# Kernel tuning notes

Measured on AMD Instinct MI355X. Metric: run time of the kernel, lower is better.

The kernel has to match this reference:

```python
import jax, jax.numpy as jnp
import numpy as np

# Hyperparameters (from init_kwargs)
N = 100000      # num_nodes
T = 4           # num_edge_type
E = 400000      # edges per type
C = 2           # num_channels
L = 2           # num_layers
W_IN = 128      # input feature dim
D = 64          # node_dim (w_out)
NUM_CLASS = 16
BETA = 0.5
M = 10000       # number of target nodes


def setup_inputs() -> dict:
    key = jax.random.key(0)
    ks = jax.random.split(key, 10)
    glorot = np.sqrt(6.0 / (W_IN + D))
    glorot1 = np.sqrt(6.0 / (C * D + D))
    glorot2 = np.sqrt(6.0 / (D + NUM_CLASS))
    return {
        "X": jax.random.normal(ks[0], (N, W_IN), dtype=jnp.float32),
        "edge_value": jax.random.uniform(ks[1], (T, E), dtype=jnp.float32),
        "conv_weights": 0.1 * jax.random.normal(ks[2], (L, C, T), dtype=jnp.float32),
        "Ws": jax.random.uniform(ks[3], (C, W_IN, D), minval=-glorot, maxval=glorot, dtype=jnp.float32),
        "lin1_w": jax.random.uniform(ks[4], (C * D, D), minval=-glorot1, maxval=glorot1, dtype=jnp.float32),
        "lin1_b": jnp.zeros((D,), dtype=jnp.float32),
        "lin_w": jax.random.uniform(ks[5], (D, NUM_CLASS), minval=-glorot2, maxval=glorot2, dtype=jnp.float32),
        "lin_b": jnp.zeros((NUM_CLASS,), dtype=jnp.float32),
        "edge_index": jax.random.randint(ks[6], (T, 2, E), 0, N),
        "target_x": jax.random.randint(ks[7], (M,), 0, N),
    }


def reference(X, edge_value, conv_weights, Ws, lin1_w, lin1_b, lin_w, lin_b,
              edge_index, target_x):
    # Flatten edge types into one big edge list. torch_sparse.coalesce(op='add')
    # followed by torch.sparse.mm is mathematically a duplicate-summing SpMM,
    # i.e. a segment_sum over destination rows.
    rows = edge_index[:, 0, :].reshape(-1)      # [T*E]
    cols = edge_index[:, 1, :].reshape(-1)      # [T*E]
    vals = edge_value.reshape(-1)               # [T*E]
    type_id = jnp.repeat(jnp.arange(T), E)      # [T*E] edge-type id (constant)

    # Per-channel input projections: X_ = X @ Ws[c]  -> [C, N, D]
    X_ = jnp.einsum('nf,cfd->cnd', X, Ws)
    H = X_

    for l in range(L):
        # FastGTConv: softmax over edge types per channel
        filt = jax.nn.softmax(conv_weights[l], axis=1)   # [C, T]
        newH = []
        for c in range(C):
            v = vals * filt[c, type_id]                  # [T*E] mixed edge weights
            msgs = v[:, None] * H[c][cols]               # gather + scale: [T*E, D]
            newH.append(jax.ops.segment_sum(msgs, rows, num_segments=N))
        H = jnp.stack(newH)                              # [C, N, D]

    # FastGTN tail: relu(beta*X_ + (1-beta)*H), concat channels, linear1
    Hc = jax.nn.relu(BETA * X_ + (1.0 - BETA) * H)       # [C, N, D]
    Hcat = jnp.transpose(Hc, (1, 0, 2)).reshape(N, C * D)
    H_ = Hcat @ lin1_w + lin1_b                          # [N, D]

    # FastGTNs head: logits at target nodes
    return H_[target_x] @ lin_w + lin_b                  # [M, NUM_CLASS]
```

## Files before the change

### kernel.cpp

```cpp
#include <hip/hip_runtime.h>

#define N_NODES   100000
#define T_TYPES   4
#define E_EDGES   400000
#define E4        100000
#define G_TOT     400000
#define C_CH      2
#define W_INF     128
#define DD        64
#define NUM_CLASS 16
#define BETA      0.5f
#define M_TGT     10000

#define NSB       1563
#define NSB_PAD   1568
#define SBPAD     1408
#define CHUNK_G   1024
#define NPART_BLK 391
#define PROJ_BLK  1563

static const size_t PLANE2 = (size_t)N_NODES * DD;

typedef __attribute__((ext_vector_type(8))) short short8x;
typedef __attribute__((ext_vector_type(4))) float f32x4;

__device__ __forceinline__ unsigned bf16rne(float x) {
    unsigned u = __float_as_uint(x);
    return (u + 0x7FFFu + ((u >> 16) & 1u)) >> 16;
}
__device__ __forceinline__ unsigned packbf(float a, float b) {
    return bf16rne(a) | (bf16rne(b) << 16);
}
__device__ __forceinline__ float bflo(unsigned u) { return __uint_as_float(u << 16); }
__device__ __forceinline__ float bfhi(unsigned u) { return __uint_as_float(u & 0xFFFF0000u); }

__device__ __forceinline__ void load_filter(const float* cw, int layer,
                                            float* f0, float* f1) {
    float m0 = -1e30f, m1 = -1e30f;
    #pragma unroll
    for (int t = 0; t < T_TYPES; ++t) {
        f0[t] = cw[layer * C_CH * T_TYPES + t];
        f1[t] = cw[layer * C_CH * T_TYPES + T_TYPES + t];
        m0 = fmaxf(m0, f0[t]); m1 = fmaxf(m1, f1[t]);
    }
    float s0 = 0.f, s1 = 0.f;
    #pragma unroll
    for (int t = 0; t < T_TYPES; ++t) {
        f0[t] = __expf(f0[t] - m0); s0 += f0[t];
        f1[t] = __expf(f1[t] - m1); s1 += f1[t];
    }
    #pragma unroll
    for (int t = 0; t < T_TYPES; ++t) { f0[t] /= s0; f1[t] /= s1; }
}

__global__ void prep_kernel(const float* __restrict__ Ws,
                            unsigned short* __restrict__ Wsb,
                            int* __restrict__ cursor) {
    int b = blockIdx.x;
    int tid = threadIdx.x;
    if (b < 64) {
        int idx = b * 256 + tid;
        int c   = idx >> 13;
        int rem = idx & 8191;
        int d   = rem >> 7;
        int k   = rem & 127;
        Wsb[idx] = (unsigned short)bf16rne(Ws[c * (W_INF * DD) + k * DD + d]);
    } else {
        int idx = (b - 64) * 256 + tid;
        if (idx < NSB) cursor[idx] = idx * SBPAD;
    }
}

__global__ __launch_bounds__(256) void build_proj_kernel(
        const int* __restrict__ edge_index,
        const float* __restrict__ edge_value,
        const float* __restrict__ cw,
        int* __restrict__ cursor,
        int2* __restrict__ edata2,
        const float* __restrict__ X,
        const unsigned short* __restrict__ Wsb,
        unsigned* __restrict__ Xp16) {
    __shared__ int cnt[NSB_PAD];
    __shared__ int gbase[NSB_PAD];
    int tid = threadIdx.x;

    if (blockIdx.x < NPART_BLK) {
        int p = blockIdx.x;
        for (int j = tid; j < NSB; j += 256) cnt[j] = 0;
        __syncthreads();

        float f0[T_TYPES], f1[T_TYPES];
        load_filter(cw, 0, f0, f1);

        int px[16], rk[16], bk[16];
        bool gv[4];
        #pragma unroll
        for (int g = 0; g < 4; ++g) {
            int idx = p * CHUNK_G + g * 256 + tid;
            gv[g] = idx < G_TOT;
            if (gv[g]) {
                int t = idx / E4, r = idx - t * E4;
                const int* bptr = edge_index + (size_t)t * 2 * E_EDGES;
                int4 rw = ((const int4*)bptr)[r];
                int4 cl = ((const int4*)(bptr + E_EDGES))[r];
                int tb = t << 17;
                int rr[4] = {rw.x, rw.y, rw.z, rw.w};
                int cc[4] = {cl.x, cl.y, cl.z, cl.w};
                #pragma unroll
                for (int k = 0; k < 4; ++k) {
                    int kk = g * 4 + k;
                    int b = rr[k] >> 6;
                    px[kk] = cc[k] | tb | ((rr[k] & 63) << 19);
                    bk[kk] = b;
                    rk[kk] = atomicAdd(&cnt[b], 1);
                }
            }
        }
        __syncthreads();
        for (int j = tid; j < NSB; j += 256)
            gbase[j] = cnt[j] ? atomicAdd(&cursor[j], cnt[j]) : 0;
        __syncthreads();
        #pragma unroll
        for (int g = 0; g < 4; ++g) {
            if (gv[g]) {
                int idx = p * CHUNK_G + g * 256 + tid;
                int t = idx / E4, r = idx - t * E4;
                float4 vv = ((const float4*)(edge_value + (size_t)t * E_EDGES))[r];
                float vf[4] = {vv.x, vv.y, vv.z, vv.w};
                #pragma unroll
                for (int k = 0; k < 4; ++k) {
                    int kk = g * 4 + k;
                    int tt = (px[kk] >> 17) & 3;
                    edata2[(size_t)gbase[bk[kk]] + rk[kk]] =
                        make_int2(px[kk], (int)packbf(vf[k] * f0[tt], vf[k] * f1[tt]));
                }
            }
        }
    } else {
        int row0 = (blockIdx.x - NPART_BLK) * 64;
        int wave = tid >> 6, lane = tid & 63;
        int m = lane & 15, q = lane >> 4;
        int arow = row0 + wave * 16 + m;
        const float4* X4 = (const float4*)X;
        union { short8x s; uint4 u; } A[4];
        bool valid = arow < N_NODES;
        #pragma unroll
        for (int ks = 0; ks < 4; ++ks) {
            float4 va = make_float4(0.f, 0.f, 0.f, 0.f), vb = va;
            if (valid) {
                va = X4[(size_t)arow * 32 + ks * 8 + q * 2];
                vb = X4[(size_t)arow * 32 + ks * 8 + q * 2 + 1];
            }
            A[ks].u = make_uint4(packbf(va.x, va.y), packbf(va.z, va.w),
                                 packbf(vb.x, vb.y), packbf(vb.z, vb.w));
        }

        #pragma unroll
        for (int ct = 0; ct < 4; ++ct) {
            f32x4 acc0 = {0.f, 0.f, 0.f, 0.f};
            f32x4 acc1 = {0.f, 0.f, 0.f, 0.f};
            #pragma unroll
            for (int ks = 0; ks < 4; ++ks) {
                short8x B0 = *(const short8x*)(Wsb + (ct * 16 + m) * 128 + ks * 32 + q * 8);
                short8x B1 = *(const short8x*)(Wsb + 8192 + (ct * 16 + m) * 128 + ks * 32 + q * 8);
                acc0 = __builtin_amdgcn_mfma_f32_16x16x32_bf16(A[ks].s, B0, acc0, 0, 0, 0);
                acc1 = __builtin_amdgcn_mfma_f32_16x16x32_bf16(A[ks].s, B1, acc1, 0, 0, 0);
            }
            #pragma unroll
            for (int r = 0; r < 4; ++r) {
                int row = row0 + wave * 16 + q * 4 + r;
                if (row < N_NODES)
                    Xp16[(size_t)row * DD + ct * 16 + m] = packbf(acc0[r], acc1[r]);
            }
        }
    }
}

__device__ __forceinline__ void qfma(const uint4 h, unsigned wp,
                                     float4& a, float4& b) {
    float w0 = bflo(wp), w1 = bfhi(wp);
    a.x = fmaf(w0, bflo(h.x), a.x);
    a.y = fmaf(w1, bfhi(h.x), a.y);
    a.z = fmaf(w0, bflo(h.y), a.z);
    a.w = fmaf(w1, bfhi(h.y), a.w);
    b.x = fmaf(w0, bflo(h.z), b.x);
    b.y = fmaf(w1, bfhi(h.z), b.y);
    b.z = fmaf(w0, bflo(h.w), b.z);
    b.w = fmaf(w1, bfhi(h.w), b.w);
}

__device__ __forceinline__ void qreduce(float4& a, float4& b) {
    a.x += __shfl_xor(a.x, 16); a.y += __shfl_xor(a.y, 16);
    a.z += __shfl_xor(a.z, 16); a.w += __shfl_xor(a.w, 16);
    b.x += __shfl_xor(b.x, 16); b.y += __shfl_xor(b.y, 16);
    b.z += __shfl_xor(b.z, 16); b.w += __shfl_xor(b.w, 16);
    a.x += __shfl_xor(a.x, 32); a.y += __shfl_xor(a.y, 32);
    a.z += __shfl_xor(a.z, 32); a.w += __shfl_xor(a.w, 32);
    b.x += __shfl_xor(b.x, 32); b.y += __shfl_xor(b.y, 32);
    b.z += __shfl_xor(b.z, 32); b.w += __shfl_xor(b.w, 32);
}

__device__ __forceinline__ int row_beg(const int* offs, int row) {
    return ((row & 63) == 0) ? (row >> 6) * SBPAD : offs[row - 1];
}

__global__ __launch_bounds__(256) void sortgather_kernel(
        const int* __restrict__ cursor,
        int2* __restrict__ edata2,
        int* __restrict__ offs,
        const unsigned* __restrict__ Hin16,
        unsigned* __restrict__ Hout16) {
    __shared__ int rcnt[64];
    __shared__ int rbase[64];
    __shared__ int rcur[64];
    __shared__ int2 ls[SBPAD];
    int tid = threadIdx.x;
    int sb = blockIdx.x;
    int base = sb * SBPAD;
    int cntb = cursor[sb] - base;

    if (tid < 64) rcnt[tid] = 0;
    __syncthreads();
    for (int j = tid; j < cntb; j += 256)
        atomicAdd(&rcnt[(edata2[base + j].x >> 19) & 63], 1);
    __syncthreads();
    if (tid < 64) {
        int c = rcnt[tid];
        int inc = c;
        #pragma unroll
        for (int off = 1; off < 64; off <<= 1) {
            int v = __shfl_up(inc, off);
            if (tid >= off) inc += v;
        }
        rbase[tid] = inc - c;
        rcur[tid]  = inc - c;
    }
    __syncthreads();
    for (int j = tid; j < cntb; j += 256) {
        int2 e = edata2[base + j];
        int pos = atomicAdd(&rcur[(e.x >> 19) & 63], 1);
        ls[pos] = e;
    }
    __syncthreads();

    for (int j = tid; j < cntb; j += 256) edata2[base + j] = ls[j];
    int row0 = sb << 6;
    if (tid < 64) {
        int row = row0 + tid;
        if (row < N_NODES) offs[row] = base + rbase[tid] + rcnt[tid];
    }

    int wv = tid >> 6, lane = tid & 63;
    int s16 = lane & 15, sub = lane >> 4;
    const uint4* hp = (const uint4*)Hin16;
    #pragma unroll 1
    for (int t16 = 0; t16 < 16; ++t16) {
        int lr = wv * 16 + t16;
        int beg = rbase[lr];
        int end = beg + rcnt[lr];
        float4 a = make_float4(0.f, 0.f, 0.f, 0.f);
        float4 b = make_float4(0.f, 0.f, 0.f, 0.f);
        int i = beg + sub;
        for (; i + 4 < end; i += 8) {
            int2 e0 = ls[i];
            int2 e1 = ls[i + 4];
            uint4 h0 = hp[(size_t)(e0.x & 0x1FFFF) * 16 + s16];
            uint4 h1 = hp[(size_t)(e1.x & 0x1FFFF) * 16 + s16];
            qfma(h0, (unsigned)e0.y, a, b);
            qfma(h1, (unsigned)e1.y, a, b);
        }
        if (i < end) {
            int2 e = ls[i];
            uint4 h = hp[(size_t)(e.x & 0x1FFFF) * 16 + s16];
            qfma(h, (unsigned)e.y, a, b);
        }
        qreduce(a, b);
        int row = row0 + lr;
        if (sub == 0 && row < N_NODES)
            ((uint4*)Hout16)[(size_t)row * 16 + s16] =
                make_uint4(packbf(a.x, a.y), packbf(a.z, a.w),
                           packbf(b.x, b.y), packbf(b.z, b.w));
    }
}

__global__ __launch_bounds__(256) void tgt_tail_kernel(const unsigned* __restrict__ Hin16,
                                                       const unsigned* __restrict__ Xp16,
                                                       const int* __restrict__ offs,
                                                       const int2* __restrict__ edata2,
                                                       const float* __restrict__ cw,
                                                       const int* __restrict__ tgt,
                                                       const float* __restrict__ lin1_w,
                                                       const float* __restrict__ lin1_b,
                                                       const float* __restrict__ lin_w,
                                                       const float* __restrict__ lin_b,
                                                       float* __restrict__ out) {
    __shared__ float l1w[W_INF * DD];
    __shared__ float lw[DD * NUM_CLASS];
    __shared__ float l1b[DD];
    __shared__ float lb[NUM_CLASS];
    __shared__ float hc[4][W_INF];
    __shared__ float hmid[4][DD];

    int tid = threadIdx.x;
    {
        const float4* g = (const float4*)lin1_w;
        float4* s = (float4*)l1w;
        #pragma unroll
        for (int i = 0; i < 8; ++i) s[tid + 256 * i] = g[tid + 256 * i];
        ((float4*)lw)[tid] = ((const float4*)lin_w)[tid];
        if (tid < DD) l1b[tid] = lin1_b[tid];
        else if (tid < DD + NUM_CLASS) lb[tid - DD] = lin_b[tid - DD];
    }

    float f0a[T_TYPES], f1a[T_TYPES], f0b[T_TYPES], f1b[T_TYPES];
    load_filter(cw, 0, f0a, f1a);
    load_filter(cw, 1, f0b, f1b);
    float r0[T_TYPES], r1[T_TYPES];
    #pragma unroll
    for (int t = 0; t < T_TYPES; ++t) { r0[t] = f0b[t] / f0a[t]; r1[t] = f1b[t] / f1a[t]; }

    int w = tid >> 6, lane = tid & 63;
    int s16 = lane & 15, sub = lane >> 4;
    int m = blockIdx.x * 4 + w;
    int row = tgt[m];
    int beg = row_beg(offs, row);
    int end = offs[row];
    const uint4* hp = (const uint4*)Hin16;
    float4 a = make_float4(0.f, 0.f, 0.f, 0.f);
    float4 b = make_float4(0.f, 0.f, 0.f, 0.f);
    for (int i = beg + sub; i < end; i += 4) {
        int2 e = edata2[i];
        int t = (e.x >> 17) & 3;
        uint4 h = hp[(size_t)(e.x & 0x1FFFF) * 16 + s16];
        unsigned wp = (unsigned)e.y;
        float w0 = bflo(wp) * r0[t], w1 = bfhi(wp) * r1[t];
        a.x = fmaf(w0, bflo(h.x), a.x);
        a.y = fmaf(w1, bfhi(h.x), a.y);
        a.z = fmaf(w0, bflo(h.y), a.z);
        a.w = fmaf(w1, bfhi(h.y), a.w);
        b.x = fmaf(w0, bflo(h.z), b.x);
        b.y = fmaf(w1, bfhi(h.z), b.y);
        b.z = fmaf(w0, bflo(h.w), b.z);
        b.w = fmaf(w1, bfhi(h.w), b.w);
    }
    qreduce(a, b);

    if (sub == 0) {
        uint4 xu = ((const uint4*)Xp16)[(size_t)row * 16 + s16];
        int d0 = 4 * s16;
        hc[w][d0 + 0]      = fmaxf(BETA * bflo(xu.x) + (1.f - BETA) * a.x, 0.f);
        hc[w][DD + d0 + 0] = fmaxf(BETA * bfhi(xu.x) + (1.f - BETA) * a.y, 0.f);
        hc[w][d0 + 1]      = fmaxf(BETA * bflo(xu.y) + (1.f - BETA) * a.z, 0.f);
        hc[w][DD + d0 + 1] = fmaxf(BETA * bfhi(xu.y) + (1.f - BETA) * a.w, 0.f);
        hc[w][d0 + 2]      = fmaxf(BETA * bflo(xu.z) + (1.f - BETA) * b.x, 0.f);
        hc[w][DD + d0 + 2] = fmaxf(BETA * bfhi(xu.z) + (1.f - BETA) * b.y, 0.f);
        hc[w][d0 + 3]      = fmaxf(BETA * bflo(xu.w) + (1.f - BETA) * b.z, 0.f);
        hc[w][DD + d0 + 3] = fmaxf(BETA * bfhi(xu.w) + (1.f - BETA) * b.w, 0.f);
    }
    __syncthreads();

    float a1 = l1b[lane];
    #pragma unroll 8
    for (int k = 0; k < W_INF; ++k)
        a1 = fmaf(hc[w][k], l1w[k * DD + lane], a1);
    hmid[w][lane] = a1;
    __syncthreads();

    if (lane < NUM_CLASS) {
        float o = lb[lane];
        #pragma unroll 8
        for (int k = 0; k < DD; ++k)
            o = fmaf(hmid[w][k], lw[k * NUM_CLASS + lane], o);
        out[(size_t)m * NUM_CLASS + lane] = o;
    }
}

extern "C" void kernel_launch(void* const* d_in, const int* in_sizes, int n_in,
                              void* d_out, int out_size, void* d_ws, size_t ws_size,
                              hipStream_t stream) {
    const float* X            = (const float*)d_in[0];
    const float* edge_value   = (const float*)d_in[1];
    const float* conv_weights = (const float*)d_in[2];
    const float* Ws           = (const float*)d_in[3];
    const float* lin1_w       = (const float*)d_in[4];
    const float* lin1_b       = (const float*)d_in[5];
    const float* lin_w        = (const float*)d_in[6];
    const float* lin_b        = (const float*)d_in[7];
    const int*   edge_index   = (const int*)d_in[8];
    const int*   target_x     = (const int*)d_in[9];
    float* out = (float*)d_out;

    unsigned*       Xp16 = (unsigned*)d_ws;
    unsigned*       H116 = Xp16 + PLANE2;
    unsigned short* Wsb  = (unsigned short*)(H116 + PLANE2);
    int*            offs = (int*)(Wsb + C_CH * W_INF * DD);
    int*            cursor = offs + N_NODES;
    int2*           edata2 = (int2*)(cursor + 1600);

    prep_kernel<<<71, 256, 0, stream>>>(Ws, Wsb, cursor);
    build_proj_kernel<<<NPART_BLK + PROJ_BLK, 256, 0, stream>>>(
        edge_index, edge_value, conv_weights, cursor, edata2, X, Wsb, Xp16);
    sortgather_kernel<<<NSB, 256, 0, stream>>>(cursor, edata2, offs, Xp16, H116);
    tgt_tail_kernel<<<M_TGT / 4, 256, 0, stream>>>(H116, Xp16, offs, edata2,
                                                   conv_weights, target_x,
                                                   lin1_w, lin1_b, lin_w, lin_b, out);
}
```

Measured before the change: 251.9 us.

## Replace two-level bucket sort with global per-row count, scan and scatter

The two-level edge sort is replaced. Before, edges were partitioned into 64-row superblocks with shared-memory atomics, then sorted per row inside the fused sort+gather kernel. Now each destination row gets a global atomic count, a per-superblock warp scan turns counts into offsets, and edges are scattered straight into CSR order with global atomics. A separate SpMM kernel then processes one row per wave. The aim is to drop the shared-memory re-sort and the serialized 16-rows-per-wave loop and to raise parallelism in the gather, at the cost of two passes of random global atomics and two extra kernel launches.

```diff
diff --git a/kernel.cpp b/kernel.cpp
--- a/kernel.cpp
+++ b/kernel.cpp
@@ -13,8 +13,8 @@
 #define M_TGT     10000
 
 #define NSB       1563
-#define NSB_PAD   1568
 #define SBPAD     1408
+#define NCNT      100032
 #define CHUNK_G   1024
 #define NPART_BLK 391
 #define PROJ_BLK  1563
@@ -55,7 +55,7 @@
 
 __global__ void prep_kernel(const float* __restrict__ Ws,
                             unsigned short* __restrict__ Wsb,
-                            int* __restrict__ cursor) {
+                            int* __restrict__ rowcnt) {
     int b = blockIdx.x;
     int tid = threadIdx.x;
     if (b < 64) {
@@ -67,73 +67,31 @@
         Wsb[idx] = (unsigned short)bf16rne(Ws[c * (W_INF * DD) + k * DD + d]);
     } else {
         int idx = (b - 64) * 256 + tid;
-        if (idx < NSB) cursor[idx] = idx * SBPAD;
-    }
-}
-
-__global__ __launch_bounds__(256) void build_proj_kernel(
+        if (idx < NCNT) rowcnt[idx] = 0;
+    }
+}
+
+__global__ __launch_bounds__(256) void count_proj_kernel(
         const int* __restrict__ edge_index,
-        const float* __restrict__ edge_value,
-        const float* __restrict__ cw,
-        int* __restrict__ cursor,
-        int2* __restrict__ edata2,
+        int* __restrict__ rowcnt,
         const float* __restrict__ X,
         const unsigned short* __restrict__ Wsb,
         unsigned* __restrict__ Xp16) {
-    __shared__ int cnt[NSB_PAD];
-    __shared__ int gbase[NSB_PAD];
     int tid = threadIdx.x;
 
     if (blockIdx.x < NPART_BLK) {
         int p = blockIdx.x;
-        for (int j = tid; j < NSB; j += 256) cnt[j] = 0;
-        __syncthreads();
-
-        float f0[T_TYPES], f1[T_TYPES];
-        load_filter(cw, 0, f0, f1);
-
-        int px[16], rk[16], bk[16];
-        bool gv[4];
         #pragma unroll
         for (int g = 0; g < 4; ++g) {
             int idx = p * CHUNK_G + g * 256 + tid;
-            gv[g] = idx < G_TOT;
-            if (gv[g]) {
+            if (idx < G_TOT) {
                 int t = idx / E4, r = idx - t * E4;
-                const int* bptr = edge_index + (size_t)t * 2 * E_EDGES;
-                int4 rw = ((const int4*)bptr)[r];
-                int4 cl = ((const int4*)(bptr + E_EDGES))[r];
-                int tb = t << 17;
-                int rr[4] = {rw.x, rw.y, rw.z, rw.w};
-                int cc[4] = {cl.x, cl.y, cl.z, cl.w};
-                #pragma unroll
-                for (int k = 0; k < 4; ++k) {
-                    int kk = g * 4 + k;
-                    int b = rr[k] >> 6;
-                    px[kk] = cc[k] | tb | ((rr[k] & 63) << 19);
-                    bk[kk] = b;
-                    rk[kk] = atomicAdd(&cnt[b], 1);
-                }
-            }
-        }
-        __syncthreads();
-        for (int j = tid; j < NSB; j += 256)
-            gbase[j] = cnt[j] ? atomicAdd(&cursor[j], cnt[j]) : 0;
-        __syncthreads();
-        #pragma unroll
-        for (int g = 0; g < 4; ++g) {
-            if (gv[g]) {
-                int idx = p * CHUNK_G + g * 256 + tid;
-                int t = idx / E4, r = idx - t * E4;
-                float4 vv = ((const float4*)(edge_value + (size_t)t * E_EDGES))[r];
-                float vf[4] = {vv.x, vv.y, vv.z, vv.w};
-                #pragma unroll
-                for (int k = 0; k < 4; ++k) {
-                    int kk = g * 4 + k;
-                    int tt = (px[kk] >> 17) & 3;
-                    edata2[(size_t)gbase[bk[kk]] + rk[kk]] =
-                        make_int2(px[kk], (int)packbf(vf[k] * f0[tt], vf[k] * f1[tt]));
-                }
+                const int4* rp = (const int4*)(edge_index + (size_t)t * 2 * E_EDGES);
+                int4 rw = rp[r];
+                atomicAdd(&rowcnt[rw.x], 1);
+                atomicAdd(&rowcnt[rw.y], 1);
+                atomicAdd(&rowcnt[rw.z], 1);
+                atomicAdd(&rowcnt[rw.w], 1);
             }
         }
     } else {
@@ -176,6 +134,62 @@
     }
 }
 
+__global__ __launch_bounds__(256) void scan_kernel(int* __restrict__ rowcnt,
+                                                   int* __restrict__ offs) {
+    int sb   = blockIdx.x * 4 + (threadIdx.x >> 6);
+    int lane = threadIdx.x & 63;
+    if (sb >= NSB) return;
+    int row = sb * 64 + lane;
+    int c = (row < N_NODES) ? rowcnt[row] : 0;
+    int inc = c;
+    #pragma unroll
+    for (int off = 1; off < 64; off <<= 1) {
+        int v = __shfl_up(inc, off);
+        if (lane >= off) inc += v;
+    }
+    int start = sb * SBPAD + inc - c;
+    if (row < N_NODES) {
+        rowcnt[row] = start;
+        offs[row]   = start + c;
+    }
+}
+
+__global__ __launch_bounds__(256) void scatter_kernel(
+        const int* __restrict__ edge_index,
+        const float* __restrict__ edge_value,
+        const float* __restrict__ cw,
+        int* __restrict__ rowcur,
+        int2* __restrict__ edata2) {
+    int tid = threadIdx.x;
+    int p = blockIdx.x;
+    float f0[T_TYPES], f1[T_TYPES];
+    load_filter(cw, 0, f0, f1);
+
+    #pragma unroll
+    for (int g = 0; g < 4; ++g) {
+        int idx = p * CHUNK_G + g * 256 + tid;
+        if (idx < G_TOT) {
+            int t = idx / E4, r = idx - t * E4;
+            const int* bptr = edge_index + (size_t)t * 2 * E_EDGES;
+            int4   rw = ((const int4*)bptr)[r];
+            int4   cl = ((const int4*)(bptr + E_EDGES))[r];
+            float4 vv = ((const float4*)(edge_value + (size_t)t * E_EDGES))[r];
+            int tb = t << 17;
+            unsigned wp = 0;
+            int   rr[4] = {rw.x, rw.y, rw.z, rw.w};
+            int   cc[4] = {cl.x, cl.y, cl.z, cl.w};
+            float vf[4] = {vv.x, vv.y, vv.z, vv.w};
+            (void)wp;
+            #pragma unroll
+            for (int k = 0; k < 4; ++k) {
+                int slot = atomicAdd(&rowcur[rr[k]], 1);
+                edata2[slot] = make_int2(cc[k] | tb,
+                                         (int)packbf(vf[k] * f0[t], vf[k] * f1[t]));
+            }
+        }
+    }
+}
+
 __device__ __forceinline__ void qfma(const uint4 h, unsigned wp,
                                      float4& a, float4& b) {
     float w0 = bflo(wp), w1 = bfhi(wp);
@@ -204,83 +218,37 @@
     return ((row & 63) == 0) ? (row >> 6) * SBPAD : offs[row - 1];
 }
 
-__global__ __launch_bounds__(256) void sortgather_kernel(
-        const int* __restrict__ cursor,
-        int2* __restrict__ edata2,
-        int* __restrict__ offs,
-        const unsigned* __restrict__ Hin16,
-        unsigned* __restrict__ Hout16) {
-    __shared__ int rcnt[64];
-    __shared__ int rbase[64];
-    __shared__ int rcur[64];
-    __shared__ int2 ls[SBPAD];
-    int tid = threadIdx.x;
-    int sb = blockIdx.x;
-    int base = sb * SBPAD;
-    int cntb = cursor[sb] - base;
-
-    if (tid < 64) rcnt[tid] = 0;
-    __syncthreads();
-    for (int j = tid; j < cntb; j += 256)
-        atomicAdd(&rcnt[(edata2[base + j].x >> 19) & 63], 1);
-    __syncthreads();
-    if (tid < 64) {
-        int c = rcnt[tid];
-        int inc = c;
-        #pragma unroll
-        for (int off = 1; off < 64; off <<= 1) {
-            int v = __shfl_up(inc, off);
-            if (tid >= off) inc += v;
-        }
-        rbase[tid] = inc - c;
-        rcur[tid]  = inc - c;
-    }
-    __syncthreads();
-    for (int j = tid; j < cntb; j += 256) {
-        int2 e = edata2[base + j];
-        int pos = atomicAdd(&rcur[(e.x >> 19) & 63], 1);
-        ls[pos] = e;
-    }
-    __syncthreads();
-
-    for (int j = tid; j < cntb; j += 256) edata2[base + j] = ls[j];
-    int row0 = sb << 6;
-    if (tid < 64) {
-        int row = row0 + tid;
-        if (row < N_NODES) offs[row] = base + rbase[tid] + rcnt[tid];
-    }
-
-    int wv = tid >> 6, lane = tid & 63;
+__global__ __launch_bounds__(256) void spmm_gather(const unsigned* __restrict__ Hin16,
+                                                   unsigned* __restrict__ Hout16,
+                                                   const int* __restrict__ offs,
+                                                   const int2* __restrict__ edata2) {
+    int lane = threadIdx.x & 63;
     int s16 = lane & 15, sub = lane >> 4;
+    int row  = (blockIdx.x * blockDim.x + threadIdx.x) >> 6;
+    int beg = row_beg(offs, row);
+    int end = offs[row];
     const uint4* hp = (const uint4*)Hin16;
-    #pragma unroll 1
-    for (int t16 = 0; t16 < 16; ++t16) {
-        int lr = wv * 16 + t16;
-        int beg = rbase[lr];
-        int end = beg + rcnt[lr];
-        float4 a = make_float4(0.f, 0.f, 0.f, 0.f);
-        float4 b = make_float4(0.f, 0.f, 0.f, 0.f);
-        int i = beg + sub;
-        for (; i + 4 < end; i += 8) {
-            int2 e0 = ls[i];
-            int2 e1 = ls[i + 4];
-            uint4 h0 = hp[(size_t)(e0.x & 0x1FFFF) * 16 + s16];
-            uint4 h1 = hp[(size_t)(e1.x & 0x1FFFF) * 16 + s16];
-            qfma(h0, (unsigned)e0.y, a, b);
-            qfma(h1, (unsigned)e1.y, a, b);
-        }
-        if (i < end) {
-            int2 e = ls[i];
-            uint4 h = hp[(size_t)(e.x & 0x1FFFF) * 16 + s16];
-            qfma(h, (unsigned)e.y, a, b);
-        }
-        qreduce(a, b);
-        int row = row0 + lr;
-        if (sub == 0 && row < N_NODES)
-            ((uint4*)Hout16)[(size_t)row * 16 + s16] =
-                make_uint4(packbf(a.x, a.y), packbf(a.z, a.w),
-                           packbf(b.x, b.y), packbf(b.z, b.w));
-    }
+    float4 a = make_float4(0.f, 0.f, 0.f, 0.f);
+    float4 b = make_float4(0.f, 0.f, 0.f, 0.f);
+    int i = beg + sub;
+    for (; i + 4 < end; i += 8) {
+        int2 e0 = edata2[i];
+        int2 e1 = edata2[i + 4];
+        uint4 h0 = hp[(size_t)(e0.x & 0x1FFFF) * 16 + s16];
+        uint4 h1 = hp[(size_t)(e1.x & 0x1FFFF) * 16 + s16];
+        qfma(h0, (unsigned)e0.y, a, b);
+        qfma(h1, (unsigned)e1.y, a, b);
+    }
+    if (i < end) {
+        int2 e = edata2[i];
+        uint4 h = hp[(size_t)(e.x & 0x1FFFF) * 16 + s16];
+        qfma(h, (unsigned)e.y, a, b);
+    }
+    qreduce(a, b);
+    if (sub == 0)
+        ((uint4*)Hout16)[(size_t)row * 16 + s16] =
+            make_uint4(packbf(a.x, a.y), packbf(a.z, a.w),
+                       packbf(b.x, b.y), packbf(b.z, b.w));
 }
 
 __global__ __launch_bounds__(256) void tgt_tail_kernel(const unsigned* __restrict__ Hin16,
@@ -394,13 +362,16 @@
     unsigned*       H116 = Xp16 + PLANE2;
     unsigned short* Wsb  = (unsigned short*)(H116 + PLANE2);
     int*            offs = (int*)(Wsb + C_CH * W_INF * DD);
-    int*            cursor = offs + N_NODES;
-    int2*           edata2 = (int2*)(cursor + 1600);
-
-    prep_kernel<<<71, 256, 0, stream>>>(Ws, Wsb, cursor);
-    build_proj_kernel<<<NPART_BLK + PROJ_BLK, 256, 0, stream>>>(
-        edge_index, edge_value, conv_weights, cursor, edata2, X, Wsb, Xp16);
-    sortgather_kernel<<<NSB, 256, 0, stream>>>(cursor, edata2, offs, Xp16, H116);
+    int*            rowcnt = offs + N_NODES;
+    int2*           edata2 = (int2*)(rowcnt + NCNT);
+
+    prep_kernel<<<64 + 391, 256, 0, stream>>>(Ws, Wsb, rowcnt);
+    count_proj_kernel<<<NPART_BLK + PROJ_BLK, 256, 0, stream>>>(
+        edge_index, rowcnt, X, Wsb, Xp16);
+    scan_kernel<<<391, 256, 0, stream>>>(rowcnt, offs);
+    scatter_kernel<<<NPART_BLK, 256, 0, stream>>>(edge_index, edge_value,
+                                                  conv_weights, rowcnt, edata2);
+    spmm_gather<<<(N_NODES * 64) / 256, 256, 0, stream>>>(Xp16, H116, offs, edata2);
     tgt_tail_kernel<<<M_TGT / 4, 256, 0, stream>>>(H116, Xp16, offs, edata2,
                                                    conv_weights, target_x,
                                                    lin1_w, lin1_b, lin_w, lin_b, out);
```

New measurement: 378.7 us. 50.3% more time.
